# Optimization experiments

Measured on AMD Instinct MI355X. Metric: run time of the kernel, lower is better.

The kernel has to match this reference:

```python
import jax, jax.numpy as jnp
import numpy as np

N_NODES = 100000
N_EDGES = 1600000
NFEAT = 256
NHID = 128
NCLASS = 8


def setup_inputs() -> dict:
    key = jax.random.key(0)
    k1, k2, k3, k4, k5 = jax.random.split(key, 5)
    x = jax.random.normal(k1, (N_NODES, NFEAT), dtype=jnp.float32)
    edge_index = jax.random.randint(k2, (2, N_EDGES), 0, N_NODES, dtype=jnp.int64)
    # GCNConv weight (glorot) and bias
    s1 = float(np.sqrt(6.0 / (NFEAT + NHID)))
    W1 = jax.random.uniform(k3, (NFEAT, NHID), dtype=jnp.float32, minval=-s1, maxval=s1)
    b1 = jnp.zeros((NHID,), dtype=jnp.float32)
    # fc Linear (xavier uniform per weights_init, bias zero)
    s2 = float(np.sqrt(6.0 / (NHID + NCLASS)))
    Wfc = jax.random.uniform(k4, (NHID, NCLASS), dtype=jnp.float32, minval=-s2, maxval=s2)
    bfc = jnp.zeros((NCLASS,), dtype=jnp.float32)
    return {"x": x, "edge_index": edge_index, "W1": W1, "b1": b1, "Wfc": Wfc, "bfc": bfc}


def gcn_conv(x, src, dst, W, b, n_nodes):
    # PyG GCNConv: h = X W; out_i = sum_j norm_ij * h_j over A+I with sym norm
    h = x @ W  # [N, nhid]
    deg = jax.ops.segment_sum(jnp.ones_like(dst, dtype=h.dtype), dst, num_segments=n_nodes)
    dinv = jnp.where(deg > 0, jax.lax.rsqrt(deg), 0.0)  # deg^{-1/2}
    norm = dinv[src] * dinv[dst]  # [E+N]
    msg = h[src] * norm[:, None]  # gather + scale, [E+N, nhid]
    out = jax.ops.segment_sum(msg, dst, num_segments=n_nodes)
    return out + b


def reference(x, edge_index, W1, b1, Wfc, bfc):
    n = x.shape[0]
    loop = jnp.arange(n, dtype=edge_index.dtype)
    src = jnp.concatenate([edge_index[0], loop])  # add self-loops
    dst = jnp.concatenate([edge_index[1], loop])
    h = gcn_conv(x, src, dst, W1, b1, n)  # GCN_Body (no activation in forward)
    return h @ Wfc + bfc  # fc
```

## Files before the change

kernel.cpp:

```cpp
#include <hip/hip_runtime.h>
#include <hip/hip_bf16.h>

#define N_NODES 100000
#define N_EDGES 1600000
#define NFEAT 256
#define NHID 128
#define NCLASS 8

#define NBLK 1024
#define BSH 8
#define BUCK 256
#define NBUCK ((N_NODES + BUCK - 1) / BUCK)
#define CAPE 6144

__global__ __launch_bounds__(256) void hist_kernel(const int* __restrict__ edst,
                                                   int* __restrict__ blockhist,
                                                   int chunk, int nE) {
    __shared__ int h[NBUCK];
    int tid = threadIdx.x;
    for (int i = tid; i < NBUCK; i += 256) h[i] = 0;
    __syncthreads();
    int e0 = blockIdx.x * chunk;
    int e1 = min(e0 + chunk, nE);
    for (int e = e0 + tid * 4; e + 3 < e1; e += 1024) {
        int4 d = *(const int4*)&edst[e];
        atomicAdd(&h[d.x >> BSH], 1);
        atomicAdd(&h[d.y >> BSH], 1);
        atomicAdd(&h[d.z >> BSH], 1);
        atomicAdd(&h[d.w >> BSH], 1);
    }
    int full = e0 + ((e1 - e0) & ~3);
    int et = full + tid;
    if (et < e1) atomicAdd(&h[edst[et] >> BSH], 1);
    __syncthreads();
    for (int i = tid; i < NBUCK; i += 256)
        blockhist[(long)blockIdx.x * NBUCK + i] = h[i];
}

__global__ __launch_bounds__(256) void scanblk_kernel(const int* __restrict__ blockhist,
                                                      int* __restrict__ blockbase,
                                                      int* __restrict__ bucket_total) {
    __shared__ int ss[256];
    int b = blockIdx.x, tid = threadIdx.x;
    int v0 = blockhist[(long)(tid * 4 + 0) * NBUCK + b];
    int v1 = blockhist[(long)(tid * 4 + 1) * NBUCK + b];
    int v2 = blockhist[(long)(tid * 4 + 2) * NBUCK + b];
    int v3 = blockhist[(long)(tid * 4 + 3) * NBUCK + b];
    int t = v0 + v1 + v2 + v3;
    ss[tid] = t; __syncthreads();
    for (int o = 1; o < 256; o <<= 1) {
        int u = (tid >= o) ? ss[tid - o] : 0;
        __syncthreads(); ss[tid] += u; __syncthreads();
    }
    int ex = ss[tid] - t;
    blockbase[(long)(tid * 4 + 0) * NBUCK + b] = ex;
    blockbase[(long)(tid * 4 + 1) * NBUCK + b] = ex + v0;
    blockbase[(long)(tid * 4 + 2) * NBUCK + b] = ex + v0 + v1;
    blockbase[(long)(tid * 4 + 3) * NBUCK + b] = ex + v0 + v1 + v2;
    if (tid == 255) bucket_total[b] = ss[255];
}

__global__ __launch_bounds__(512) void mid_kernel(const int* __restrict__ bucket_total,
                                                  int* __restrict__ bucket_base,
                                                  const float* __restrict__ W1,
                                                  const float* __restrict__ b1,
                                                  const float* __restrict__ Wfc,
                                                  const float* __restrict__ bfc,
                                                  float* __restrict__ WcT,
                                                  float* __restrict__ cvec) {
    int tid = threadIdx.x;
    if (blockIdx.x == 0) {
        __shared__ int ss[512];
        int v = (tid < NBUCK) ? bucket_total[tid] : 0;
        ss[tid] = v; __syncthreads();
        for (int o = 1; o < 512; o <<= 1) {
            int u = (tid >= o) ? ss[tid - o] : 0;
            __syncthreads(); ss[tid] += u; __syncthreads();
        }
        if (tid < NBUCK) bucket_base[tid] = ss[tid] - v;
        if (tid == NBUCK - 1) bucket_base[NBUCK] = ss[tid];
    } else {
        __shared__ float wfs[NHID * NCLASS];
        __shared__ float bs[NHID];
        for (int i = tid; i < NHID * NCLASS; i += 512) wfs[i] = Wfc[i];
        if (tid < NHID) bs[tid] = b1[tid];
        __syncthreads();
        if (tid < NFEAT) {
            float acc[NCLASS] = {};
            for (int h = 0; h < NHID; h++) {
                float w = W1[tid * NHID + h];
                #pragma unroll
                for (int c = 0; c < NCLASS; c++) acc[c] += w * wfs[h * NCLASS + c];
            }
            #pragma unroll
            for (int c = 0; c < NCLASS; c++) WcT[c * NFEAT + tid] = acc[c];
        }
        if (tid < NCLASS) {
            float a = bfc[tid];
            for (int h = 0; h < NHID; h++) a += bs[h] * wfs[h * NCLASS + tid];
            cvec[tid] = a;
        }
    }
}

__global__ __launch_bounds__(256) void scat_kernel(const int* __restrict__ esrc,
                                                   const int* __restrict__ edst,
                                                   const int* __restrict__ blockbase,
                                                   const int* __restrict__ bucket_base,
                                                   int* __restrict__ ebufP,
                                                   int chunk, int nE) {
    __shared__ int cur[NBUCK];
    int tid = threadIdx.x;
    for (int i = tid; i < NBUCK; i += 256)
        cur[i] = bucket_base[i] + blockbase[(long)blockIdx.x * NBUCK + i];
    __syncthreads();
    int e0 = blockIdx.x * chunk;
    int e1 = min(e0 + chunk, nE);
    for (int e = e0 + tid * 4; e + 3 < e1; e += 1024) {
        int4 s = *(const int4*)&esrc[e];
        int4 d = *(const int4*)&edst[e];
        int p0 = atomicAdd(&cur[d.x >> BSH], 1);
        int p1 = atomicAdd(&cur[d.y >> BSH], 1);
        int p2 = atomicAdd(&cur[d.z >> BSH], 1);
        int p3 = atomicAdd(&cur[d.w >> BSH], 1);
        ebufP[p0] = (s.x << BSH) | (d.x & (BUCK - 1));
        ebufP[p1] = (s.y << BSH) | (d.y & (BUCK - 1));
        ebufP[p2] = (s.z << BSH) | (d.z & (BUCK - 1));
        ebufP[p3] = (s.w << BSH) | (d.w & (BUCK - 1));
    }
    int full = e0 + ((e1 - e0) & ~3);
    int et = full + tid;
    if (et < e1) {
        int s = esrc[et], d = edst[et];
        int pos = atomicAdd(&cur[d >> BSH], 1);
        ebufP[pos] = (s << BSH) | (d & (BUCK - 1));
    }
}

__global__ __launch_bounds__(512) void deg_dinv_kernel(const int* __restrict__ ebufP,
                                                       const int* __restrict__ bucket_base,
                                                       float* __restrict__ dinv) {
    __shared__ int cnt[BUCK];
    int b = blockIdx.x, tid = threadIdx.x;
    if (tid < BUCK) cnt[tid] = 0;
    __syncthreads();
    int base = bucket_base[b], end = bucket_base[b + 1];
    int a0 = min((base + 3) & ~3, end);
    if (base + tid < a0) atomicAdd(&cnt[ebufP[base + tid] & (BUCK - 1)], 1);
    for (int e = a0 + tid * 4; e + 3 < end; e += 2048) {
        int4 p = *(const int4*)&ebufP[e];
        atomicAdd(&cnt[p.x & (BUCK - 1)], 1);
        atomicAdd(&cnt[p.y & (BUCK - 1)], 1);
        atomicAdd(&cnt[p.z & (BUCK - 1)], 1);
        atomicAdd(&cnt[p.w & (BUCK - 1)], 1);
    }
    int full = a0 + ((end - a0) & ~3);
    int et = full + tid;
    if (et < end) atomicAdd(&cnt[ebufP[et] & (BUCK - 1)], 1);
    __syncthreads();
    if (tid < BUCK) {
        int node = (b << BSH) + tid;
        if (node < N_NODES) dinv[node] = rsqrtf((float)(cnt[tid] + 1));
    }
}

__global__ __launch_bounds__(256) void z_kernel(const float* __restrict__ X,
                                                const float* __restrict__ WcT,
                                                const float* __restrict__ dinv,
                                                float* __restrict__ Zs, int n) {
    __shared__ float4 wlds[NCLASS * 64];
    int tid = threadIdx.x;
    #pragma unroll
    for (int i = tid; i < NCLASS * 64; i += 256)
        wlds[i] = ((const float4*)WcT)[i];
    __syncthreads();

    const int lane = tid & 63;
    const int sub  = lane & 7;
    const int rsub = lane >> 3;
    const int wid  = (blockIdx.x * 256 + tid) >> 6;
    const int nw   = (gridDim.x * 256) >> 6;
    const int ngroups = (n + 7) >> 3;

    for (int g = wid; g < ngroups; g += nw) {
        int row = g * 8 + rsub;
        bool ok = row < n;
        int r = ok ? row : (n - 1);
        const float4* xr = (const float4*)(X + (long)r * NFEAT);
        float4 xv[8];
        #pragma unroll
        for (int k = 0; k < 8; k++) xv[k] = xr[sub + 8 * k];

        float res = 0.f;
        #pragma unroll
        for (int c = 0; c < NCLASS; c++) {
            float s = 0.f;
            #pragma unroll
            for (int k = 0; k < 8; k++) {
                float4 w = wlds[c * 64 + sub + 8 * k];
                s += xv[k].x * w.x + xv[k].y * w.y + xv[k].z * w.z + xv[k].w * w.w;
            }
            s += __shfl_xor(s, 1);
            s += __shfl_xor(s, 2);
            s += __shfl_xor(s, 4);
            if (sub == c) res = s;
        }
        if (ok) Zs[(long)row * NCLASS + sub] = res * dinv[row];
    }
}

__global__ __launch_bounds__(512) void sort_gather_kernel(
        const float* __restrict__ Zs,
        const int* __restrict__ ebufP,
        const int* __restrict__ bucket_base,
        const float* __restrict__ cvec,
        float* __restrict__ out, int n) {
    __shared__ int cnt[BUCK];
    __shared__ int off[BUCK + 1];
    __shared__ int ss[BUCK];
    __shared__ int sorted[CAPE];
    int b = blockIdx.x, tid = threadIdx.x;
    int base = bucket_base[b], end = bucket_base[b + 1];
    int total = end - base;
    const float4* Zs4 = (const float4*)Zs;
    float4 c0v = ((const float4*)cvec)[0];
    float4 c1v = ((const float4*)cvec)[1];

    if (total <= CAPE) {
        if (tid < BUCK) cnt[tid] = 0;
        __syncthreads();
        int a0 = min((base + 3) & ~3, end);
        if (base + tid < a0) atomicAdd(&cnt[ebufP[base + tid] & (BUCK - 1)], 1);
        for (int e = a0 + tid * 4; e + 3 < end; e += 2048) {
            int4 p = *(const int4*)&ebufP[e];
            atomicAdd(&cnt[p.x & (BUCK - 1)], 1);
            atomicAdd(&cnt[p.y & (BUCK - 1)], 1);
            atomicAdd(&cnt[p.z & (BUCK - 1)], 1);
            atomicAdd(&cnt[p.w & (BUCK - 1)], 1);
        }
        int full = a0 + ((end - a0) & ~3);
        if (full + tid < end) atomicAdd(&cnt[ebufP[full + tid] & (BUCK - 1)], 1);
        __syncthreads();

        int t = (tid < BUCK) ? cnt[tid] : 0;
        if (tid < BUCK) ss[tid] = t;
        __syncthreads();
        for (int o = 1; o < BUCK; o <<= 1) {
            int u = 0;
            if (tid < BUCK && tid >= o) u = ss[tid - o];
            __syncthreads();
            if (tid < BUCK) ss[tid] += u;
            __syncthreads();
        }
        if (tid < BUCK) {
            off[tid] = ss[tid] - t;
            cnt[tid] = ss[tid] - t;
            if (tid == BUCK - 1) off[BUCK] = ss[tid];
        }
        __syncthreads();

        if (base + tid < a0) {
            int p = ebufP[base + tid];
            int slot = atomicAdd(&cnt[p & (BUCK - 1)], 1);
            sorted[slot] = p >> BSH;
        }
        for (int e = a0 + tid * 4; e + 3 < end; e += 2048) {
            int4 p = *(const int4*)&ebufP[e];
            int s0 = atomicAdd(&cnt[p.x & (BUCK - 1)], 1);
            int s1 = atomicAdd(&cnt[p.y & (BUCK - 1)], 1);
            int s2 = atomicAdd(&cnt[p.z & (BUCK - 1)], 1);
            int s3 = atomicAdd(&cnt[p.w & (BUCK - 1)], 1);
            sorted[s0] = p.x >> BSH;
            sorted[s1] = p.y >> BSH;
            sorted[s2] = p.z >> BSH;
            sorted[s3] = p.w >> BSH;
        }
        if (full + tid < end) {
            int p = ebufP[full + tid];
            int slot = atomicAdd(&cnt[p & (BUCK - 1)], 1);
            sorted[slot] = p >> BSH;
        }
        __syncthreads();

        int li = tid >> 1;
        int h  = tid & 1;
        int node = (b << BSH) + li;
        if (node < n) {
            int k0 = off[li], k1 = off[li + 1];
            float4 a = Zs4[node * 2 + h];
            int k = k0;
            for (; k + 1 < k1; k += 2) {
                int s0 = sorted[k], s1 = sorted[k + 1];
                float4 z0 = Zs4[s0 * 2 + h];
                float4 z1 = Zs4[s1 * 2 + h];
                a.x += z0.x + z1.x; a.y += z0.y + z1.y;
                a.z += z0.z + z1.z; a.w += z0.w + z1.w;
            }
            if (k < k1) {
                float4 z = Zs4[sorted[k] * 2 + h];
                a.x += z.x; a.y += z.y; a.z += z.z; a.w += z.w;
            }
            float dd = rsqrtf((float)(k1 - k0 + 1));
            float4 cv = h ? c1v : c0v;
            float4 o;
            o.x = a.x * dd + cv.x; o.y = a.y * dd + cv.y;
            o.z = a.z * dd + cv.z; o.w = a.w * dd + cv.w;
            ((float4*)out)[node * 2 + h] = o;
        }
    } else {
        float* acc = (float*)sorted;
        __shared__ int dcount[BUCK];
        if (tid < BUCK) dcount[tid] = 0;
        for (int i = tid; i < NCLASS * BUCK; i += 512) acc[i] = 0.f;
        __syncthreads();
        for (int e = base + tid; e < end; e += 512) {
            int p = ebufP[e];
            int src = p >> BSH;
            int li = p & (BUCK - 1);
            atomicAdd(&dcount[li], 1);
            float4 z0 = Zs4[src * 2];
            float4 z1 = Zs4[src * 2 + 1];
            atomicAdd(&acc[0 * BUCK + li], z0.x);
            atomicAdd(&acc[1 * BUCK + li], z0.y);
            atomicAdd(&acc[2 * BUCK + li], z0.z);
            atomicAdd(&acc[3 * BUCK + li], z0.w);
            atomicAdd(&acc[4 * BUCK + li], z1.x);
            atomicAdd(&acc[5 * BUCK + li], z1.y);
            atomicAdd(&acc[6 * BUCK + li], z1.z);
            atomicAdd(&acc[7 * BUCK + li], z1.w);
        }
        __syncthreads();
        if (tid < BUCK) {
            int node = (b << BSH) + tid;
            if (node < n) {
                float4 s0 = Zs4[node * 2];
                float4 s1 = Zs4[node * 2 + 1];
                float dd = rsqrtf((float)(dcount[tid] + 1));
                float4 o0, o1;
                o0.x = (s0.x + acc[0 * BUCK + tid]) * dd + c0v.x;
                o0.y = (s0.y + acc[1 * BUCK + tid]) * dd + c0v.y;
                o0.z = (s0.z + acc[2 * BUCK + tid]) * dd + c0v.z;
                o0.w = (s0.w + acc[3 * BUCK + tid]) * dd + c0v.w;
                o1.x = (s1.x + acc[4 * BUCK + tid]) * dd + c1v.x;
                o1.y = (s1.y + acc[5 * BUCK + tid]) * dd + c1v.y;
                o1.z = (s1.z + acc[6 * BUCK + tid]) * dd + c1v.z;
                o1.w = (s1.w + acc[7 * BUCK + tid]) * dd + c1v.w;
                ((float4*)out)[node * 2]     = o0;
                ((float4*)out)[node * 2 + 1] = o1;
            }
        }
    }
}

extern "C" void kernel_launch(void* const* d_in, const int* in_sizes, int n_in,
                              void* d_out, int out_size, void* d_ws, size_t ws_size,
                              hipStream_t stream) {
    const float* x    = (const float*)d_in[0];
    const int*   eidx = (const int*)d_in[1];
    const float* W1   = (const float*)d_in[2];
    const float* b1   = (const float*)d_in[3];
    const float* Wfc  = (const float*)d_in[4];
    const float* bfc  = (const float*)d_in[5];
    float* out = (float*)d_out;

    const int N = N_NODES;
    const int E = in_sizes[1] / 2;
    const int chunk = (((E + NBLK - 1) / NBLK) + 3) & ~3;

    const int* esrc = eidx;
    const int* edst = eidx + E;

    float* Zs    = (float*)d_ws;
    float* dinv  = Zs + (long)8 * N;
    float* cvec  = dinv + N;
    float* WcT   = cvec + 8;
    int*   btot  = (int*)(WcT + NCLASS * NFEAT);
    int*   bbase = btot + NBUCK + 1;
    int*   bhist = bbase + NBUCK + 4;
    int*   bbas2 = bhist + (long)NBLK * NBUCK;
    size_t ofs = (size_t)(bbas2 + (long)NBLK * NBUCK - (int*)d_ws);
    ofs = (ofs + 3) & ~(size_t)3;
    int*   ebufP = (int*)d_ws + ofs;

    hist_kernel<<<NBLK, 256, 0, stream>>>(edst, bhist, chunk, E);
    scanblk_kernel<<<NBUCK, 256, 0, stream>>>(bhist, bbas2, btot);
    mid_kernel<<<2, 512, 0, stream>>>(btot, bbase, W1, b1, Wfc, bfc, WcT, cvec);
    scat_kernel<<<NBLK, 256, 0, stream>>>(esrc, edst, bbas2, bbase, ebufP, chunk, E);
    deg_dinv_kernel<<<NBUCK, 512, 0, stream>>>(ebufP, bbase, dinv);
    z_kernel<<<1563, 256, 0, stream>>>(x, WcT, dinv, Zs, N);
    sort_gather_kernel<<<NBUCK, 512, 0, stream>>>(Zs, ebufP, bbase, cvec, out, N);
}
```

Before: 236.6 us.

## Fuse edge bucketing into one pass with fixed-capacity buckets and atomic cursors

The separate histogram, block-scan and bucket-base-scan kernels are replaced with a single scatter kernel. It builds a per-block local histogram, reserves space in fixed-capacity (CAPB) global buckets through atomic cursors, stages edges sorted in LDS, and writes each bucket contiguously. Node degrees are now counted with global atomics in the same pass, so the separate degree kernel is removed and z_kernel computes rsqrt inline. The dense-accumulation fallback for oversized buckets is dropped, so any bucket above capacity would be silently truncated; that holds only for fairly uniform edge distributions.

Result: slower. 282.4 us (+19.3%).

```diff
diff --git a/kernel.cpp b/kernel.cpp
--- a/kernel.cpp
+++ b/kernel.cpp
@@ -1,85 +1,23 @@
 #include <hip/hip_runtime.h>
-#include <hip/hip_bf16.h>
 
 #define N_NODES 100000
-#define N_EDGES 1600000
 #define NFEAT 256
 #define NHID 128
 #define NCLASS 8
 
-#define NBLK 1024
 #define BSH 8
 #define BUCK 256
 #define NBUCK ((N_NODES + BUCK - 1) / BUCK)
-#define CAPE 6144
-
-__global__ __launch_bounds__(256) void hist_kernel(const int* __restrict__ edst,
-                                                   int* __restrict__ blockhist,
-                                                   int chunk, int nE) {
-    __shared__ int h[NBUCK];
-    int tid = threadIdx.x;
-    for (int i = tid; i < NBUCK; i += 256) h[i] = 0;
-    __syncthreads();
-    int e0 = blockIdx.x * chunk;
-    int e1 = min(e0 + chunk, nE);
-    for (int e = e0 + tid * 4; e + 3 < e1; e += 1024) {
-        int4 d = *(const int4*)&edst[e];
-        atomicAdd(&h[d.x >> BSH], 1);
-        atomicAdd(&h[d.y >> BSH], 1);
-        atomicAdd(&h[d.z >> BSH], 1);
-        atomicAdd(&h[d.w >> BSH], 1);
-    }
-    int full = e0 + ((e1 - e0) & ~3);
-    int et = full + tid;
-    if (et < e1) atomicAdd(&h[edst[et] >> BSH], 1);
-    __syncthreads();
-    for (int i = tid; i < NBUCK; i += 256)
-        blockhist[(long)blockIdx.x * NBUCK + i] = h[i];
-}
-
-__global__ __launch_bounds__(256) void scanblk_kernel(const int* __restrict__ blockhist,
-                                                      int* __restrict__ blockbase,
-                                                      int* __restrict__ bucket_total) {
-    __shared__ int ss[256];
-    int b = blockIdx.x, tid = threadIdx.x;
-    int v0 = blockhist[(long)(tid * 4 + 0) * NBUCK + b];
-    int v1 = blockhist[(long)(tid * 4 + 1) * NBUCK + b];
-    int v2 = blockhist[(long)(tid * 4 + 2) * NBUCK + b];
-    int v3 = blockhist[(long)(tid * 4 + 3) * NBUCK + b];
-    int t = v0 + v1 + v2 + v3;
-    ss[tid] = t; __syncthreads();
-    for (int o = 1; o < 256; o <<= 1) {
-        int u = (tid >= o) ? ss[tid - o] : 0;
-        __syncthreads(); ss[tid] += u; __syncthreads();
-    }
-    int ex = ss[tid] - t;
-    blockbase[(long)(tid * 4 + 0) * NBUCK + b] = ex;
-    blockbase[(long)(tid * 4 + 1) * NBUCK + b] = ex + v0;
-    blockbase[(long)(tid * 4 + 2) * NBUCK + b] = ex + v0 + v1;
-    blockbase[(long)(tid * 4 + 3) * NBUCK + b] = ex + v0 + v1 + v2;
-    if (tid == 255) bucket_total[b] = ss[255];
-}
-
-__global__ __launch_bounds__(512) void mid_kernel(const int* __restrict__ bucket_total,
-                                                  int* __restrict__ bucket_base,
-                                                  const float* __restrict__ W1,
-                                                  const float* __restrict__ b1,
-                                                  const float* __restrict__ Wfc,
-                                                  const float* __restrict__ bfc,
-                                                  float* __restrict__ WcT,
-                                                  float* __restrict__ cvec) {
+#define CAPB 5120
+#define NBLK1 512
+#define CHMAX 3200
+
+__global__ __launch_bounds__(512) void init_kernel(const float* __restrict__ W1,
+        const float* __restrict__ b1, const float* __restrict__ Wfc,
+        const float* __restrict__ bfc, float* __restrict__ WcT,
+        float* __restrict__ cvec, int* __restrict__ deg, int* __restrict__ gcur) {
     int tid = threadIdx.x;
     if (blockIdx.x == 0) {
-        __shared__ int ss[512];
-        int v = (tid < NBUCK) ? bucket_total[tid] : 0;
-        ss[tid] = v; __syncthreads();
-        for (int o = 1; o < 512; o <<= 1) {
-            int u = (tid >= o) ? ss[tid - o] : 0;
-            __syncthreads(); ss[tid] += u; __syncthreads();
-        }
-        if (tid < NBUCK) bucket_base[tid] = ss[tid] - v;
-        if (tid == NBUCK - 1) bucket_base[NBUCK] = ss[tid];
-    } else {
         __shared__ float wfs[NHID * NCLASS];
         __shared__ float bs[NHID];
         for (int i = tid; i < NHID * NCLASS; i += 512) wfs[i] = Wfc[i];
@@ -100,73 +38,91 @@
             for (int h = 0; h < NHID; h++) a += bs[h] * wfs[h * NCLASS + tid];
             cvec[tid] = a;
         }
+    } else {
+        int i = (blockIdx.x - 1) * 512 + tid;
+        if (i < N_NODES) deg[i] = 0;
+        if (blockIdx.x == 1 && tid < NBUCK) gcur[tid] = tid * CAPB;
     }
 }
 
 __global__ __launch_bounds__(256) void scat_kernel(const int* __restrict__ esrc,
-                                                   const int* __restrict__ edst,
-                                                   const int* __restrict__ blockbase,
-                                                   const int* __restrict__ bucket_base,
-                                                   int* __restrict__ ebufP,
-                                                   int chunk, int nE) {
-    __shared__ int cur[NBUCK];
+        const int* __restrict__ edst, int* __restrict__ deg, int* __restrict__ gcur,
+        int* __restrict__ ebufP, int chunk, int nE) {
+    __shared__ int h[NBUCK + 1];
+    __shared__ int lbase[NBUCK + 1];
+    __shared__ int lcur[NBUCK];
+    __shared__ int ssc[256];
+    __shared__ int pk[CHMAX];
+    __shared__ unsigned short bk[CHMAX];
     int tid = threadIdx.x;
-    for (int i = tid; i < NBUCK; i += 256)
-        cur[i] = bucket_base[i] + blockbase[(long)blockIdx.x * NBUCK + i];
+    for (int i = tid; i < NBUCK + 1; i += 256) h[i] = 0;
     __syncthreads();
     int e0 = blockIdx.x * chunk;
     int e1 = min(e0 + chunk, nE);
+    int cntE = e1 - e0;
+    for (int e = e0 + tid * 4; e + 3 < e1; e += 1024) {
+        int4 d = *(const int4*)&edst[e];
+        atomicAdd(&h[d.x >> BSH], 1); atomicAdd(&h[d.y >> BSH], 1);
+        atomicAdd(&h[d.z >> BSH], 1); atomicAdd(&h[d.w >> BSH], 1);
+        atomicAdd(&deg[d.x], 1); atomicAdd(&deg[d.y], 1);
+        atomicAdd(&deg[d.z], 1); atomicAdd(&deg[d.w], 1);
+    }
+    int full = e0 + (cntE & ~3);
+    if (full + tid < e1) {
+        int d = edst[full + tid];
+        atomicAdd(&h[d >> BSH], 1);
+        atomicAdd(&deg[d], 1);
+    }
+    __syncthreads();
+    int i0 = 2 * tid, i1 = 2 * tid + 1;
+    int v0 = (i0 <= NBUCK) ? h[i0] : 0;
+    int v1 = (i1 <= NBUCK) ? h[i1] : 0;
+    ssc[tid] = v0 + v1;
+    __syncthreads();
+    for (int o = 1; o < 256; o <<= 1) {
+        int u = (tid >= o) ? ssc[tid - o] : 0;
+        __syncthreads(); ssc[tid] += u; __syncthreads();
+    }
+    int ex = ssc[tid] - (v0 + v1);
+    if (i0 <= NBUCK) lbase[i0] = ex;
+    if (i1 <= NBUCK) lbase[i1] = ex + v0;
+    __syncthreads();
+    for (int b = tid; b < NBUCK; b += 256) {
+        int c = h[b];
+        int gb = c ? atomicAdd(&gcur[b], c) : 0;
+        h[b] = gb;
+        lcur[b] = lbase[b];
+    }
+    __syncthreads();
     for (int e = e0 + tid * 4; e + 3 < e1; e += 1024) {
         int4 s = *(const int4*)&esrc[e];
         int4 d = *(const int4*)&edst[e];
-        int p0 = atomicAdd(&cur[d.x >> BSH], 1);
-        int p1 = atomicAdd(&cur[d.y >> BSH], 1);
-        int p2 = atomicAdd(&cur[d.z >> BSH], 1);
-        int p3 = atomicAdd(&cur[d.w >> BSH], 1);
-        ebufP[p0] = (s.x << BSH) | (d.x & (BUCK - 1));
-        ebufP[p1] = (s.y << BSH) | (d.y & (BUCK - 1));
-        ebufP[p2] = (s.z << BSH) | (d.z & (BUCK - 1));
-        ebufP[p3] = (s.w << BSH) | (d.w & (BUCK - 1));
-    }
-    int full = e0 + ((e1 - e0) & ~3);
-    int et = full + tid;
-    if (et < e1) {
-        int s = esrc[et], d = edst[et];
-        int pos = atomicAdd(&cur[d >> BSH], 1);
-        ebufP[pos] = (s << BSH) | (d & (BUCK - 1));
-    }
-}
-
-__global__ __launch_bounds__(512) void deg_dinv_kernel(const int* __restrict__ ebufP,
-                                                       const int* __restrict__ bucket_base,
-                                                       float* __restrict__ dinv) {
-    __shared__ int cnt[BUCK];
-    int b = blockIdx.x, tid = threadIdx.x;
-    if (tid < BUCK) cnt[tid] = 0;
-    __syncthreads();
-    int base = bucket_base[b], end = bucket_base[b + 1];
-    int a0 = min((base + 3) & ~3, end);
-    if (base + tid < a0) atomicAdd(&cnt[ebufP[base + tid] & (BUCK - 1)], 1);
-    for (int e = a0 + tid * 4; e + 3 < end; e += 2048) {
-        int4 p = *(const int4*)&ebufP[e];
-        atomicAdd(&cnt[p.x & (BUCK - 1)], 1);
-        atomicAdd(&cnt[p.y & (BUCK - 1)], 1);
-        atomicAdd(&cnt[p.z & (BUCK - 1)], 1);
-        atomicAdd(&cnt[p.w & (BUCK - 1)], 1);
-    }
-    int full = a0 + ((end - a0) & ~3);
-    int et = full + tid;
-    if (et < end) atomicAdd(&cnt[ebufP[et] & (BUCK - 1)], 1);
-    __syncthreads();
-    if (tid < BUCK) {
-        int node = (b << BSH) + tid;
-        if (node < N_NODES) dinv[node] = rsqrtf((float)(cnt[tid] + 1));
+        int b0 = d.x >> BSH, b1_ = d.y >> BSH, b2 = d.z >> BSH, b3 = d.w >> BSH;
+        int p0 = atomicAdd(&lcur[b0], 1);
+        int p1 = atomicAdd(&lcur[b1_], 1);
+        int p2 = atomicAdd(&lcur[b2], 1);
+        int p3 = atomicAdd(&lcur[b3], 1);
+        pk[p0] = (s.x << BSH) | (d.x & (BUCK - 1)); bk[p0] = (unsigned short)b0;
+        pk[p1] = (s.y << BSH) | (d.y & (BUCK - 1)); bk[p1] = (unsigned short)b1_;
+        pk[p2] = (s.z << BSH) | (d.z & (BUCK - 1)); bk[p2] = (unsigned short)b2;
+        pk[p3] = (s.w << BSH) | (d.w & (BUCK - 1)); bk[p3] = (unsigned short)b3;
+    }
+    if (full + tid < e1) {
+        int s = esrc[full + tid], d = edst[full + tid];
+        int b = d >> BSH;
+        int p = atomicAdd(&lcur[b], 1);
+        pk[p] = (s << BSH) | (d & (BUCK - 1)); bk[p] = (unsigned short)b;
+    }
+    __syncthreads();
+    for (int i = tid; i < cntE; i += 256) {
+        int b = bk[i];
+        ebufP[h[b] + (i - lbase[b])] = pk[i];
     }
 }
 
 __global__ __launch_bounds__(256) void z_kernel(const float* __restrict__ X,
                                                 const float* __restrict__ WcT,
-                                                const float* __restrict__ dinv,
+                                                const int* __restrict__ deg,
                                                 float* __restrict__ Zs, int n) {
     __shared__ float4 wlds[NCLASS * 64];
     int tid = threadIdx.x;
@@ -205,150 +161,109 @@
             s += __shfl_xor(s, 4);
             if (sub == c) res = s;
         }
-        if (ok) Zs[(long)row * NCLASS + sub] = res * dinv[row];
+        if (ok) {
+            float dv = rsqrtf((float)(deg[row] + 1));
+            Zs[(long)row * NCLASS + sub] = res * dv;
+        }
     }
 }
 
 __global__ __launch_bounds__(512) void sort_gather_kernel(
         const float* __restrict__ Zs,
         const int* __restrict__ ebufP,
-        const int* __restrict__ bucket_base,
+        const int* __restrict__ gcur,
         const float* __restrict__ cvec,
         float* __restrict__ out, int n) {
     __shared__ int cnt[BUCK];
     __shared__ int off[BUCK + 1];
     __shared__ int ss[BUCK];
-    __shared__ int sorted[CAPE];
+    __shared__ int sorted[CAPB];
     int b = blockIdx.x, tid = threadIdx.x;
-    int base = bucket_base[b], end = bucket_base[b + 1];
-    int total = end - base;
+    int base = b * CAPB;
+    int end = min(gcur[b], base + CAPB);
     const float4* Zs4 = (const float4*)Zs;
     float4 c0v = ((const float4*)cvec)[0];
     float4 c1v = ((const float4*)cvec)[1];
 
-    if (total <= CAPE) {
-        if (tid < BUCK) cnt[tid] = 0;
+    if (tid < BUCK) cnt[tid] = 0;
+    __syncthreads();
+    int a0 = min((base + 3) & ~3, end);
+    if (base + tid < a0) atomicAdd(&cnt[ebufP[base + tid] & (BUCK - 1)], 1);
+    for (int e = a0 + tid * 4; e + 3 < end; e += 2048) {
+        int4 p = *(const int4*)&ebufP[e];
+        atomicAdd(&cnt[p.x & (BUCK - 1)], 1);
+        atomicAdd(&cnt[p.y & (BUCK - 1)], 1);
+        atomicAdd(&cnt[p.z & (BUCK - 1)], 1);
+        atomicAdd(&cnt[p.w & (BUCK - 1)], 1);
+    }
+    int full = a0 + ((end - a0) & ~3);
+    if (full + tid < end) atomicAdd(&cnt[ebufP[full + tid] & (BUCK - 1)], 1);
+    __syncthreads();
+
+    int t = (tid < BUCK) ? cnt[tid] : 0;
+    if (tid < BUCK) ss[tid] = t;
+    __syncthreads();
+    for (int o = 1; o < BUCK; o <<= 1) {
+        int u = 0;
+        if (tid < BUCK && tid >= o) u = ss[tid - o];
         __syncthreads();
-        int a0 = min((base + 3) & ~3, end);
-        if (base + tid < a0) atomicAdd(&cnt[ebufP[base + tid] & (BUCK - 1)], 1);
-        for (int e = a0 + tid * 4; e + 3 < end; e += 2048) {
-            int4 p = *(const int4*)&ebufP[e];
-            atomicAdd(&cnt[p.x & (BUCK - 1)], 1);
-            atomicAdd(&cnt[p.y & (BUCK - 1)], 1);
-            atomicAdd(&cnt[p.z & (BUCK - 1)], 1);
-            atomicAdd(&cnt[p.w & (BUCK - 1)], 1);
-        }
-        int full = a0 + ((end - a0) & ~3);
-        if (full + tid < end) atomicAdd(&cnt[ebufP[full + tid] & (BUCK - 1)], 1);
+        if (tid < BUCK) ss[tid] += u;
         __syncthreads();
-
-        int t = (tid < BUCK) ? cnt[tid] : 0;
-        if (tid < BUCK) ss[tid] = t;
-        __syncthreads();
-        for (int o = 1; o < BUCK; o <<= 1) {
-            int u = 0;
-            if (tid < BUCK && tid >= o) u = ss[tid - o];
-            __syncthreads();
-            if (tid < BUCK) ss[tid] += u;
-            __syncthreads();
-        }
-        if (tid < BUCK) {
-            off[tid] = ss[tid] - t;
-            cnt[tid] = ss[tid] - t;
-            if (tid == BUCK - 1) off[BUCK] = ss[tid];
-        }
-        __syncthreads();
-
-        if (base + tid < a0) {
-            int p = ebufP[base + tid];
-            int slot = atomicAdd(&cnt[p & (BUCK - 1)], 1);
-            sorted[slot] = p >> BSH;
-        }
-        for (int e = a0 + tid * 4; e + 3 < end; e += 2048) {
-            int4 p = *(const int4*)&ebufP[e];
-            int s0 = atomicAdd(&cnt[p.x & (BUCK - 1)], 1);
-            int s1 = atomicAdd(&cnt[p.y & (BUCK - 1)], 1);
-            int s2 = atomicAdd(&cnt[p.z & (BUCK - 1)], 1);
-            int s3 = atomicAdd(&cnt[p.w & (BUCK - 1)], 1);
-            sorted[s0] = p.x >> BSH;
-            sorted[s1] = p.y >> BSH;
-            sorted[s2] = p.z >> BSH;
-            sorted[s3] = p.w >> BSH;
-        }
-        if (full + tid < end) {
-            int p = ebufP[full + tid];
-            int slot = atomicAdd(&cnt[p & (BUCK - 1)], 1);
-            sorted[slot] = p >> BSH;
-        }
-        __syncthreads();
-
-        int li = tid >> 1;
-        int h  = tid & 1;
-        int node = (b << BSH) + li;
-        if (node < n) {
-            int k0 = off[li], k1 = off[li + 1];
-            float4 a = Zs4[node * 2 + h];
-            int k = k0;
-            for (; k + 1 < k1; k += 2) {
-                int s0 = sorted[k], s1 = sorted[k + 1];
-                float4 z0 = Zs4[s0 * 2 + h];
-                float4 z1 = Zs4[s1 * 2 + h];
-                a.x += z0.x + z1.x; a.y += z0.y + z1.y;
-                a.z += z0.z + z1.z; a.w += z0.w + z1.w;
-            }
-            if (k < k1) {
-                float4 z = Zs4[sorted[k] * 2 + h];
-                a.x += z.x; a.y += z.y; a.z += z.z; a.w += z.w;
-            }
-            float dd = rsqrtf((float)(k1 - k0 + 1));
-            float4 cv = h ? c1v : c0v;
-            float4 o;
-            o.x = a.x * dd + cv.x; o.y = a.y * dd + cv.y;
-            o.z = a.z * dd + cv.z; o.w = a.w * dd + cv.w;
-            ((float4*)out)[node * 2 + h] = o;
-        }
-    } else {
-        float* acc = (float*)sorted;
-        __shared__ int dcount[BUCK];
-        if (tid < BUCK) dcount[tid] = 0;
-        for (int i = tid; i < NCLASS * BUCK; i += 512) acc[i] = 0.f;
-        __syncthreads();
-        for (int e = base + tid; e < end; e += 512) {
-            int p = ebufP[e];
-            int src = p >> BSH;
-            int li = p & (BUCK - 1);
-            atomicAdd(&dcount[li], 1);
-            float4 z0 = Zs4[src * 2];
-            float4 z1 = Zs4[src * 2 + 1];
-            atomicAdd(&acc[0 * BUCK + li], z0.x);
-            atomicAdd(&acc[1 * BUCK + li], z0.y);
-            atomicAdd(&acc[2 * BUCK + li], z0.z);
-            atomicAdd(&acc[3 * BUCK + li], z0.w);
-            atomicAdd(&acc[4 * BUCK + li], z1.x);
-            atomicAdd(&acc[5 * BUCK + li], z1.y);
-            atomicAdd(&acc[6 * BUCK + li], z1.z);
-            atomicAdd(&acc[7 * BUCK + li], z1.w);
-        }
-        __syncthreads();
-        if (tid < BUCK) {
-            int node = (b << BSH) + tid;
-            if (node < n) {
-                float4 s0 = Zs4[node * 2];
-                float4 s1 = Zs4[node * 2 + 1];
-                float dd = rsqrtf((float)(dcount[tid] + 1));
-                float4 o0, o1;
-                o0.x = (s0.x + acc[0 * BUCK + tid]) * dd + c0v.x;
-                o0.y = (s0.y + acc[1 * BUCK + tid]) * dd + c0v.y;
-                o0.z = (s0.z + acc[2 * BUCK + tid]) * dd + c0v.z;
-                o0.w = (s0.w + acc[3 * BUCK + tid]) * dd + c0v.w;
-                o1.x = (s1.x + acc[4 * BUCK + tid]) * dd + c1v.x;
-                o1.y = (s1.y + acc[5 * BUCK + tid]) * dd + c1v.y;
-                o1.z = (s1.z + acc[6 * BUCK + tid]) * dd + c1v.z;
-                o1.w = (s1.w + acc[7 * BUCK + tid]) * dd + c1v.w;
-                ((float4*)out)[node * 2]     = o0;
-                ((float4*)out)[node * 2 + 1] = o1;
-            }
-        }
+    }
+    if (tid < BUCK) {
+        off[tid] = ss[tid] - t;
+        cnt[tid] = ss[tid] - t;
+        if (tid == BUCK - 1) off[BUCK] = ss[tid];
+    }
+    __syncthreads();
+
+    if (base + tid < a0) {
+        int p = ebufP[base + tid];
+        int slot = atomicAdd(&cnt[p & (BUCK - 1)], 1);
+        sorted[slot] = p >> BSH;
+    }
+    for (int e = a0 + tid * 4; e + 3 < end; e += 2048) {
+        int4 p = *(const int4*)&ebufP[e];
+        int s0 = atomicAdd(&cnt[p.x & (BUCK - 1)], 1);
+        int s1 = atomicAdd(&cnt[p.y & (BUCK - 1)], 1);
+        int s2 = atomicAdd(&cnt[p.z & (BUCK - 1)], 1);
+        int s3 = atomicAdd(&cnt[p.w & (BUCK - 1)], 1);
+        sorted[s0] = p.x >> BSH;
+        sorted[s1] = p.y >> BSH;
+        sorted[s2] = p.z >> BSH;
+        sorted[s3] = p.w >> BSH;
+    }
+    if (full + tid < end) {
+        int p = ebufP[full + tid];
+        int slot = atomicAdd(&cnt[p & (BUCK - 1)], 1);
+        sorted[slot] = p >> BSH;
+    }
+    __syncthreads();
+
+    int li = tid >> 1;
+    int hh = tid & 1;
+    int node = (b << BSH) + li;
+    if (node < n) {
+        int k0 = off[li], k1 = off[li + 1];
+        float4 a = Zs4[node * 2 + hh];
+        int k = k0;
+        for (; k + 1 < k1; k += 2) {
+            int s0 = sorted[k], s1 = sorted[k + 1];
+            float4 z0 = Zs4[s0 * 2 + hh];
+            float4 z1 = Zs4[s1 * 2 + hh];
+            a.x += z0.x + z1.x; a.y += z0.y + z1.y;
+            a.z += z0.z + z1.z; a.w += z0.w + z1.w;
+        }
+        if (k < k1) {
+            float4 z = Zs4[sorted[k] * 2 + hh];
+            a.x += z.x; a.y += z.y; a.z += z.z; a.w += z.w;
+        }
+        float dd = rsqrtf((float)(k1 - k0 + 1));
+        float4 cv = hh ? c1v : c0v;
+        float4 o;
+        o.x = a.x * dd + cv.x; o.y = a.y * dd + cv.y;
+        o.z = a.z * dd + cv.z; o.w = a.w * dd + cv.w;
+        ((float4*)out)[node * 2 + hh] = o;
     }
 }
 
@@ -365,28 +280,21 @@
 
     const int N = N_NODES;
     const int E = in_sizes[1] / 2;
-    const int chunk = (((E + NBLK - 1) / NBLK) + 3) & ~3;
 
     const int* esrc = eidx;
     const int* edst = eidx + E;
 
     float* Zs    = (float*)d_ws;
-    float* dinv  = Zs + (long)8 * N;
-    float* cvec  = dinv + N;
+    float* cvec  = Zs + (long)8 * N;
     float* WcT   = cvec + 8;
-    int*   btot  = (int*)(WcT + NCLASS * NFEAT);
-    int*   bbase = btot + NBUCK + 1;
-    int*   bhist = bbase + NBUCK + 4;
-    int*   bbas2 = bhist + (long)NBLK * NBUCK;
-    size_t ofs = (size_t)(bbas2 + (long)NBLK * NBUCK - (int*)d_ws);
-    ofs = (ofs + 3) & ~(size_t)3;
-    int*   ebufP = (int*)d_ws + ofs;
-
-    hist_kernel<<<NBLK, 256, 0, stream>>>(edst, bhist, chunk, E);
-    scanblk_kernel<<<NBUCK, 256, 0, stream>>>(bhist, bbas2, btot);
-    mid_kernel<<<2, 512, 0, stream>>>(btot, bbase, W1, b1, Wfc, bfc, WcT, cvec);
-    scat_kernel<<<NBLK, 256, 0, stream>>>(esrc, edst, bbas2, bbase, ebufP, chunk, E);
-    deg_dinv_kernel<<<NBUCK, 512, 0, stream>>>(ebufP, bbase, dinv);
-    z_kernel<<<1563, 256, 0, stream>>>(x, WcT, dinv, Zs, N);
-    sort_gather_kernel<<<NBUCK, 512, 0, stream>>>(Zs, ebufP, bbase, cvec, out, N);
-}
+    int*   deg   = (int*)(WcT + NCLASS * NFEAT);
+    int*   gcur  = deg + N;
+    int*   ebufP = gcur + 392;
+
+    const int chunk = (((E + NBLK1 - 1) / NBLK1) + 3) & ~3;
+
+    init_kernel<<<1 + (N + 511) / 512, 512, 0, stream>>>(W1, b1, Wfc, bfc, WcT, cvec, deg, gcur);
+    scat_kernel<<<NBLK1, 256, 0, stream>>>(esrc, edst, deg, gcur, ebufP, chunk, E);
+    z_kernel<<<1563, 256, 0, stream>>>(x, WcT, deg, Zs, N);
+    sort_gather_kernel<<<NBUCK, 512, 0, stream>>>(Zs, ebufP, gcur, cvec, out, N);
+}
```
